# Performance work log

Measured on AMD Instinct MI355X. Metric: run time of the kernel, lower is better.

Reference implementation:

```python
import jax, jax.numpy as jnp
import numpy as np

N = 50000       # nodes
E = 1600000     # edges
H = 64          # hidden_channels
G = 16          # graphs in batch
DOUT = 2        # dim_out
NODE_IN = 1
EDGE_IN = 3


def setup_inputs() -> dict:
    key = jax.random.key(0)
    ks = jax.random.split(key, 24)
    p = lambda k, shape: (jax.random.normal(k, shape, jnp.float32) * 0.05)
    inp = {
        "x": jax.random.normal(ks[0], (N, NODE_IN), jnp.float32),
        "edge_index": jax.random.randint(ks[1], (2, E), 0, N, dtype=jnp.int64),
        "edge_attr": jax.random.normal(ks[2], (E, EDGE_IN), jnp.float32),
        "batch": jnp.sort(jax.random.randint(ks[3], (N,), 0, G, dtype=jnp.int64)),
        # EdgeModel MLP: Linear(2*node_in+edge_in, H), ReLU, Linear(H, H)
        "ew1": p(ks[4], (2 * NODE_IN + EDGE_IN, H)), "eb1": p(ks[5], (H,)),
        "ew2": p(ks[6], (H, H)), "eb2": p(ks[7], (H,)),
        # NodeModel MLP: Linear(node_in+edge_out, H), ReLU, Linear(H, H)
        "nw1": p(ks[8], (NODE_IN + H, H)), "nb1": p(ks[9], (H,)),
        "nw2": p(ks[10], (H, H)), "nb2": p(ks[11], (H,)),
        "ow1": p(ks[12], (H, H)), "ob1": p(ks[13], (H,)),
        "ow2": p(ks[14], (H, H)), "ob2": p(ks[15], (H,)),
        "ow3": p(ks[16], (H, H)), "ob3": p(ks[17], (H,)),
        "ow4": p(ks[18], (H, DOUT)), "ob4": p(ks[19], (DOUT,)),
    }
    return inp


def reference(x, edge_index, edge_attr, batch,
              ew1, eb1, ew2, eb2,
              nw1, nb1, nw2, nb2,
              ow1, ob1, ow2, ob2, ow3, ob3, ow4, ob4):
    row, col = edge_index[0], edge_index[1]
    # EdgeModel: gather endpoints, concat, 2-layer MLP (no residual)
    e_in = jnp.concatenate([x[row], x[col], edge_attr], axis=1)      # [E, 2+3]
    e = jax.nn.relu(e_in @ ew1 + eb1) @ ew2 + eb2                    # [E, H]
    # NodeModel: scatter_add edge messages into destination nodes
    agg = jax.ops.segment_sum(e, col, num_segments=x.shape[0])      # [N, H]
    h_in = jnp.concatenate([x, agg], axis=1)                         # [N, 1+H]
    h = jax.nn.relu(h_in @ nw1 + nb1) @ nw2 + nb2                    # [N, H]
    # global_add_pool over graphs
    pooled = jax.ops.segment_sum(h, batch, num_segments=G)          # [G, H]
    o = jax.nn.relu(pooled @ ow1 + ob1)
    o = jax.nn.relu(o @ ow2 + ob2)
    o = jax.nn.relu(o @ ow3 + ob3)
    return o @ ow4 + ob4                                             # [G, DOUT]
```

## Files before the change

### kernel.cpp

```cpp
#include <hip/hip_runtime.h>
#include <hip/hip_bf16.h>

#define HID 64
#define NGRAPH 16
#define BN 32
#define GB 8
#define MAXNB 2048
#define NCB 256
#define NCT 1024
#define SORT_T 1024
#define SORT_CHUNK 12800

typedef __attribute__((ext_vector_type(8))) short short8;
typedef __attribute__((ext_vector_type(4))) float f32x4;

enum : int {
  OFF_V      = 1040,
  OFF_M      = 1104,
  OFF_EW1    = 5200,
  OFF_EB1    = 5520,
  OFF_NW1    = 5584,
  OFF_NB1    = 9744,
  OFF_NW2    = 9808,
  OFF_NB2    = 13904,
  OFF_OW1    = 13968,
  OFF_OB1    = 18064,
  OFF_OW2    = 18128,
  OFF_OB2    = 22224,
  OFF_OW3    = 22288,
  OFF_OB3    = 26384,
  OFF_OW4    = 26448,
  OFF_OB4    = 26576,
  OFF_EW2    = 26578,
  OFF_EB2    = 30674,
  OFF_FLAGS  = 30738,
  OFF_W1T    = 30740,
  OFF_MT     = 30996,
  OFF_PREP   = 33044
};

struct WPtrs { const void* p[16]; };

__device__ __forceinline__ float cv(float v) { return v; }
__device__ __forceinline__ float cv(__hip_bfloat16 v) { return __bfloat162float(v); }
__device__ __forceinline__ unsigned short f2bu(float v) {
  union { __hip_bfloat16 b; unsigned short u; } c;
  c.b = __float2bfloat16(v);
  return c.u;
}
__device__ __forceinline__ unsigned short fr(float v) {
  unsigned u = __float_as_uint(v);
  u += 0x7FFFu + ((u >> 16) & 1u);
  return (unsigned short)(u >> 16);
}
__device__ __forceinline__ unsigned rndpack(float a, float b) {
  unsigned ua = __float_as_uint(fmaxf(a, 0.0f));
  unsigned ub = __float_as_uint(fmaxf(b, 0.0f));
  ua += 0x7FFFu + ((ua >> 16) & 1u);
  ub += 0x7FFFu + ((ub >> 16) & 1u);
  return __builtin_amdgcn_perm(ub, ua, 0x07060302u);
}

__global__ __launch_bounds__(256) void prep_kernel(
    const void* xv, const void* eiv, WPtrs wp, float* ws)
{
  __shared__ int red[2];
  __shared__ int s_ft;
  __shared__ float ew2s[4096];
  __shared__ float nw1s[4096];
  const int t = threadIdx.x;

  if (t == 0) { red[0] = 0; red[1] = 0; }
  __syncthreads();
  {
    const unsigned* u = (const unsigned*)xv;
    int big = 0;
    for (int i = t; i < 512; i += 256) {
      const unsigned el = (u[i] >> 7) & 0xFFu;
      big += (el >= 140u) ? 1 : 0;
    }
    atomicAdd(&red[0], big);
  }
  {
    const int* e32 = (const int*)eiv;
    int orv = 0;
    for (int i = 1 + 2 * t; i < 2048; i += 512) orv |= e32[i];
    atomicOr(&red[1], orv);
  }
  __syncthreads();
  if (t == 0) {
    const int ft = (red[0] < 8) ? 1 : 0;
    const int it = (red[1] == 0) ? 1 : 0;
    ((int*)(ws + OFF_FLAGS))[0] = ft;
    ((int*)(ws + OFF_FLAGS))[1] = it;
    s_ft = ft;
  }
  __syncthreads();
  const int ft = s_ft;

  const int sz[16]  = {320,64,4096,64,4160,64,4096,64,4096,64,4096,64,4096,64,128,2};
  const int dst[16] = {OFF_EW1,OFF_EB1,OFF_EW2,OFF_EB2,OFF_NW1,OFF_NB1,OFF_NW2,OFF_NB2,
                       OFF_OW1,OFF_OB1,OFF_OW2,OFF_OB2,OFF_OW3,OFF_OB3,OFF_OW4,OFF_OB4};
  for (int a = 0; a < 16; ++a) {
    const void* src = wp.p[a];
    float* d = ws + dst[a];
    const int n = sz[a];
    for (int i = t; i < n; i += 256)
      d[i] = ft ? __bfloat162float(((const __hip_bfloat16*)src)[i])
                : ((const float*)src)[i];
  }
  __syncthreads();

  for (int i = t; i < 4096; i += 256) {
    ew2s[i] = ws[OFF_EW2 + i];
    nw1s[i] = ws[OFF_NW1 + 64 + i];
  }
  __syncthreads();
  for (int idx = t; idx < 4096; idx += 256) {
    const int i = idx >> 6, j = idx & 63;
    float s = 0.0f;
    #pragma unroll 8
    for (int k = 0; k < 64; ++k)
      s = fmaf(ew2s[i * 64 + k], nw1s[k * 64 + j], s);
    ws[OFF_M + idx] = s;
  }
  for (int j = t; j < 64; j += 256) {
    float s = 0.0f;
    #pragma unroll 8
    for (int k = 0; k < 64; ++k)
      s = fmaf(ws[OFF_EB2 + k], nw1s[k * 64 + j], s);
    ws[OFF_V + j] = s;
  }
  __syncthreads();

  unsigned short* w1t = (unsigned short*)(ws + OFF_W1T);
  for (int n = t; n < 64; n += 256) {
    #pragma unroll
    for (int k = 0; k < 8; ++k) {
      float v = 0.0f;
      if (k < 5) v = ws[OFF_EW1 + k * 64 + n];
      else if (k == 5) v = ws[OFF_EB1 + n];
      w1t[n * 8 + k] = f2bu(v);
    }
  }
  unsigned short* mt = (unsigned short*)(ws + OFF_MT);
  for (int idx = t; idx < 4096; idx += 256) {
    const int n = idx >> 6, k = idx & 63;
    mt[idx] = f2bu(ws[OFF_M + k * 64 + n]);
  }
}

template<typename IT>
__device__ __forceinline__ void count_impl(
    const IT* __restrict__ ei, const IT* __restrict__ bt,
    int* __restrict__ gcnt, int* __restrict__ endG, int* lh,
    const int E, const int N, const int NBG)
{
  const int t = threadIdx.x;
  const int b = blockIdx.x;
  for (int i = t; i < NBG; i += NCT) lh[i] = 0;
  {
    const int i = b * NCT + t;
    if (i < N) {
      const int g1 = (int)bt[i];
      if (i == 0) for (int g = 0; g < g1; ++g) endG[g] = 0;
      if (i == N - 1) {
        for (int g = g1; g < NGRAPH; ++g) endG[g] = N;
      } else {
        const int g2 = (int)bt[i + 1];
        for (int g = g1; g < g2; ++g) endG[g] = i + 1;
      }
    }
  }
  __syncthreads();
  const int per = (E + NCB - 1) / NCB;
  const int a = b * per;
  const int bnd = (a + per < E) ? (a + per) : E;
  for (int e = a + t; e < bnd; e += NCT) {
    const int c = (int)ei[(size_t)E + e];
    atomicAdd(&lh[c >> 8], 1);
  }
  __syncthreads();
  for (int i = t; i < NBG; i += NCT) gcnt[(size_t)i * NCB + b] = lh[i];
}

__global__ __launch_bounds__(NCT) void count_kernel(
    const void* eiv, const void* batv, const float* ws,
    int* gcnt, int* endG, const int E, const int N, const int NBG)
{
  __shared__ int lh[MAXNB];
  const int it = ((const int*)(ws + OFF_FLAGS))[1];
  if (it) count_impl<long long>((const long long*)eiv, (const long long*)batv, gcnt, endG, lh, E, N, NBG);
  else    count_impl<int>((const int*)eiv, (const int*)batv, gcnt, endG, lh, E, N, NBG);
}

__global__ __launch_bounds__(256) void scan_tot_kernel(
    const int* __restrict__ gcnt, int* __restrict__ gstart, const int NBG)
{
  const int lane = threadIdx.x & 63;
  const int bkt = blockIdx.x * 4 + (threadIdx.x >> 6);
  if (bkt >= NBG) return;
  const int4 v = *(const int4*)(gcnt + (size_t)bkt * NCB + lane * 4);
  int s = v.x + v.y + v.z + v.w;
  #pragma unroll
  for (int off = 32; off > 0; off >>= 1) s += __shfl_xor(s, off);
  if (lane == 0) gstart[bkt] = s;
}

__global__ __launch_bounds__(256) void scan_pref_kernel(
    int* __restrict__ gstart, const int NBG)
{
  __shared__ int ps[256];
  const int t = threadIdx.x;
  const int seg = (NBG + 255) / 256;
  int s = 0;
  for (int i = 0; i < seg; ++i) {
    const int idx = t * seg + i;
    if (idx < NBG) s += gstart[idx];
  }
  ps[t] = s;
  __syncthreads();
  for (int off = 1; off < 256; off <<= 1) {
    const int v = (t >= off) ? ps[t - off] : 0;
    __syncthreads();
    ps[t] += v;
    __syncthreads();
  }
  int carry = ps[t] - s;
  for (int i = 0; i < seg; ++i) {
    const int idx = t * seg + i;
    if (idx < NBG) {
      const int c = gstart[idx];
      gstart[idx] = carry;
      carry += c;
    }
  }
  if (t == 255) gstart[NBG] = ps[255];
}

__global__ __launch_bounds__(256) void scan_row_kernel(
    int* __restrict__ gcnt, const int* __restrict__ gstart, const int NBG)
{
  const int lane = threadIdx.x & 63;
  const int bkt = blockIdx.x * 4 + (threadIdx.x >> 6);
  if (bkt >= NBG) return;
  int* row = gcnt + (size_t)bkt * NCB;
  const int4 v = *(const int4*)(row + lane * 4);
  const int ls = v.x + v.y + v.z + v.w;
  int s = ls;
  #pragma unroll
  for (int off = 1; off < 64; off <<= 1) {
    const int u = __shfl_up(s, off);
    if (lane >= off) s += u;
  }
  int e = s - ls + gstart[bkt];
  int4 o;
  o.x = e; e += v.x;
  o.y = e; e += v.y;
  o.z = e; e += v.z;
  o.w = e;
  *(int4*)(row + lane * 4) = o;
}

template<typename FT, typename IT>
__device__ __forceinline__ void scatter_impl(
    const FT* __restrict__ x, const IT* __restrict__ ei, const FT* __restrict__ ea,
    const int* __restrict__ gcnt, const int* __restrict__ gstart,
    ushort4* __restrict__ recB, unsigned char* __restrict__ cid, int* lb,
    const int E, const int gb0, const int gb1, const int cap)
{
  const int t = threadIdx.x;
  const int b = blockIdx.x;
  __shared__ int sbase;
  if (t == 0) sbase = gstart[gb0];
  __syncthreads();
  const int base = sbase;
  const int gcount = gb1 - gb0;
  for (int i = t; i < gcount; i += NCT) lb[i] = gcnt[(size_t)(gb0 + i) * NCB + b] - base;
  __syncthreads();

  const int per = (E + NCB - 1) / NCB;
  const int a = b * per;
  const int bnd = (a + per < E) ? (a + per) : E;
  for (int e = a + t; e < bnd; e += NCT) {
    const int c = (int)ei[(size_t)E + e];
    const int grp = c >> 8;
    if (grp >= gb0 && grp < gb1) {
      const int pos = atomicAdd(&lb[grp - gb0], 1);
      if (pos < cap) {
        const int r = (int)ei[e];
        ushort4 rv;
        rv.x = fr(cv(x[r]));
        rv.y = fr(cv(ea[(size_t)3 * e + 0]));
        rv.z = fr(cv(ea[(size_t)3 * e + 1]));
        rv.w = fr(cv(ea[(size_t)3 * e + 2]));
        recB[pos] = rv;
        cid[pos] = (unsigned char)(c & 255);
      }
    }
  }
}

__global__ __launch_bounds__(NCT) void scatter_kernel(
    const void* xv, const void* eiv, const void* eav, const float* ws,
    const int* gcnt, const int* gstart, ushort4* recB, unsigned char* cid,
    const int E, const int gb0, const int gb1, const int cap)
{
  __shared__ int lb[MAXNB];
  const int* fl = (const int*)(ws + OFF_FLAGS);
  const int ft = fl[0], it = fl[1];
  if (ft) {
    if (it) scatter_impl<__hip_bfloat16, long long>((const __hip_bfloat16*)xv, (const long long*)eiv, (const __hip_bfloat16*)eav, gcnt, gstart, recB, cid, lb, E, gb0, gb1, cap);
    else    scatter_impl<__hip_bfloat16, int>((const __hip_bfloat16*)xv, (const int*)eiv, (const __hip_bfloat16*)eav, gcnt, gstart, recB, cid, lb, E, gb0, gb1, cap);
  } else {
    if (it) scatter_impl<float, long long>((const float*)xv, (const long long*)eiv, (const float*)eav, gcnt, gstart, recB, cid, lb, E, gb0, gb1, cap);
    else    scatter_impl<float, int>((const float*)xv, (const int*)eiv, (const float*)eav, gcnt, gstart, recB, cid, lb, E, gb0, gb1, cap);
  }
}

__global__ __launch_bounds__(SORT_T) void sort_kernel(
    ushort4* __restrict__ recB, unsigned char* __restrict__ cid,
    const int* __restrict__ gstart, int* __restrict__ bstartF,
    const int NB, const int gr0, const int cap)
{
  __shared__ unsigned sru[SORT_CHUNK * 2];
  __shared__ unsigned char sc[SORT_CHUNK];
  __shared__ int h2[16][GB];
  __shared__ int fs[GB];
  __shared__ int cur[GB];

  const int t = threadIdx.x;
  const int lane = t & 63;
  const int wav = t >> 6;
  const int g = gr0 + (int)blockIdx.x;

  const int base0 = gstart[gr0];
  int rb = gstart[g] - base0;
  int re = gstart[g + 1] - base0;
  if (rb > cap) rb = cap;
  if (re > cap) re = cap;
  int cnt = re - rb;
  if (cnt > SORT_CHUNK) cnt = SORT_CHUNK;

  if (t < 16 * GB) ((int*)h2)[t] = 0;
  __syncthreads();

  for (int i = t; i < cnt; i += SORT_T) {
    const ushort4 r = recB[rb + i];
    sru[2 * i]     = (unsigned)r.x | ((unsigned)r.y << 16);
    sru[2 * i + 1] = (unsigned)r.z | ((unsigned)r.w << 16);
    const unsigned char c = cid[rb + i];
    sc[i] = c;
    const int kk = c >> 5;
    unsigned long long mym = 0;
    #pragma unroll
    for (int k = 0; k < GB; ++k) {
      const unsigned long long bk = __ballot(kk == k);
      if (kk == k) mym = bk;
    }
    if ((mym & (((unsigned long long)1 << lane) - 1ull)) == 0)
      h2[wav][kk] += (int)__builtin_popcountll(mym);
  }
  __syncthreads();

  if (t == 0) {
    int acc = 0;
    for (int k = 0; k < GB; ++k) {
      int s = 0;
      #pragma unroll
      for (int w = 0; w < 16; ++w) s += h2[w][k];
      fs[k] = acc;
      cur[k] = acc;
      acc += s;
    }
  }
  __syncthreads();

  if (t <= GB) {
    const int bk = g * GB + t;
    if (bk <= NB) bstartF[bk] = base0 + rb + ((t == GB) ? cnt : fs[t]);
  }

  for (int i = t; i < cnt; i += SORT_T) {
    const unsigned char c = sc[i];
    const int kk = c >> 5;
    unsigned long long mym = 0;
    #pragma unroll
    for (int k = 0; k < GB; ++k) {
      const unsigned long long bk = __ballot(kk == k);
      if (kk == k) mym = bk;
    }
    const int lead = (int)__builtin_ctzll(mym);
    const int off = (int)__builtin_popcountll(mym & (((unsigned long long)1 << lane) - 1ull));
    int bas = 0;
    if (lane == lead) bas = atomicAdd(&cur[kk], (int)__builtin_popcountll(mym));
    bas = __shfl(bas, lead);
    const int pos = rb + bas + off;
    const unsigned a = sru[2 * i], b = sru[2 * i + 1];
    ushort4 rv;
    rv.x = (unsigned short)(a & 0xFFFFu); rv.y = (unsigned short)(a >> 16);
    rv.z = (unsigned short)(b & 0xFFFFu); rv.w = (unsigned short)(b >> 16);
    recB[pos] = rv;
    cid[pos] = (unsigned char)(c & 31);
  }
}

template<typename FT, typename IT>
__device__ __forceinline__ void fused_impl(
    const FT* __restrict__ x, const IT* __restrict__ batch,
    const float* __restrict__ ws, const int* __restrict__ bstart,
    const ushort4* __restrict__ recB, const unsigned char* __restrict__ cid,
    float* __restrict__ rep,
    short* sA, unsigned char* scid, short* sHT, short* aggB,
    float* pooledL, float* xls, unsigned short* xlsb, int* sbi,
    const int N, const int gb0, const int cap)
{
  const int t = threadIdx.x;
  const int lane = t & 63;
  const int quad = lane >> 4;
  const int l15 = lane & 15;
  const int wav = t >> 6;
  const int bucket = gb0 + blockIdx.x;

  for (int i = t; i < NGRAPH * 64; i += 256) pooledL[i] = 0.0f;
  if (t < BN) {
    const int n = bucket * BN + t;
    const float xvv = (n < N) ? cv(x[n]) : 0.0f;
    xls[t] = xvv;
    xlsb[t] = fr(xvv);
  }
  if (t == 0) {
    const int nf = bucket * BN, nl = bucket * BN + BN - 1;
    sbi[0] = (int)batch[(nf < N) ? nf : (N - 1)];
    sbi[1] = (int)batch[(nl < N) ? nl : (N - 1)];
    sbi[2] = bstart[gb0];
  }
  __syncthreads();

  const unsigned short* w1t = (const unsigned short*)(ws + OFF_W1T);
  short8 B1[4];
  #pragma unroll
  for (int tn = 0; tn < 4; ++tn) {
    short8 z; for (int j = 0; j < 8; ++j) z[j] = 0;
    if (quad == 0) z = *(const short8*)(w1t + (16 * tn + l15) * 8);
    B1[tn] = z;
  }
  short8 ONES8;
  #pragma unroll
  for (int j = 0; j < 8; ++j) ONES8[j] = (short)0x3F80;

  const int base = sbi[2];
  int s0 = bstart[bucket] - base;
  int e0 = bstart[bucket + 1] - base;
  if (s0 > cap) s0 = cap;
  if (e0 > cap) e0 = cap;

  f32x4 C2[2]; C2[0] = (f32x4)0.0f; C2[1] = (f32x4)0.0f;
  f32x4 C3[2]; C3[0] = (f32x4)0.0f; C3[1] = (f32x4)0.0f;

  const int nedge = e0 - s0;
  const int nst = (nedge + 255) >> 8;
  for (int st = 0; st < nst; ++st) {
    {
      const int idx = s0 + st * 256 + t;
      const bool valid = idx < e0;
      ushort4 rv = valid ? recB[idx] : make_ushort4(0, 0, 0, 0);
      const int c = valid ? (int)cid[idx] : 255;
      short8 row;
      row[0] = (short)rv.x;
      row[1] = valid ? (short)xlsb[c] : (short)0;
      row[2] = (short)rv.y; row[3] = (short)rv.z; row[4] = (short)rv.w;
      row[5] = valid ? (short)0x3F80 : (short)0;
      row[6] = 0; row[7] = 0;
      *(short8*)(sA + t * 8) = row;
      scid[t] = (unsigned char)c;
    }
    __syncthreads();

    const int m = nedge - st * 256;
    const int jmax = (m >= 256) ? 4 : ((m + 63) >> 6);
    for (int j = 0; j < jmax; ++j) {
      short* HT = sHT + (j & 1) * (64 * 72);
      short8 a1;
      if (quad == 0) a1 = *(const short8*)(sA + (j * 64 + 16 * wav + l15) * 8);
      else { for (int jj = 0; jj < 8; ++jj) a1[jj] = 0; }
      f32x4 Hc[4];
      #pragma unroll
      for (int tn = 0; tn < 4; ++tn)
        Hc[tn] = __builtin_amdgcn_mfma_f32_16x16x32_bf16(a1, B1[tn], (f32x4)0.0f, 0, 0, 0);
      #pragma unroll
      for (int tn = 0; tn < 4; ++tn) {
        uint2 pk;
        pk.x = rndpack(Hc[tn][0], Hc[tn][1]);
        pk.y = rndpack(Hc[tn][2], Hc[tn][3]);
        *(uint2*)(HT + (16 * tn + l15) * 72 + 16 * wav + quad * 4) = pk;
      }
      __syncthreads();

      const unsigned* sp = (const unsigned*)(scid + j * 64);
      #pragma unroll
      for (int q = 0; q < 2; ++q) {
        const unsigned lo = sp[2 * quad + 8 * q];
        const unsigned hi = sp[2 * quad + 8 * q + 1];
        short8 a2[2];
        #pragma unroll
        for (int tm2 = 0; tm2 < 2; ++tm2) {
          const int seg = 16 * tm2 + l15;
          short8 v;
          v[0] = (((lo      ) & 255u) == (unsigned)seg) ? (short)0x3F80 : (short)0;
          v[1] = (((lo >>  8) & 255u) == (unsigned)seg) ? (short)0x3F80 : (short)0;
          v[2] = (((lo >> 16) & 255u) == (unsigned)seg) ? (short)0x3F80 : (short)0;
          v[3] = (((lo >> 24) & 255u) == (unsigned)seg) ? (short)0x3F80 : (short)0;
          v[4] = (((hi      ) & 255u) == (unsigned)seg) ? (short)0x3F80 : (short)0;
          v[5] = (((hi >>  8) & 255u) == (unsigned)seg) ? (short)0x3F80 : (short)0;
          v[6] = (((hi >> 16) & 255u) == (unsigned)seg) ? (short)0x3F80 : (short)0;
          v[7] = (((hi >> 24) & 255u) == (unsigned)seg) ? (short)0x3F80 : (short)0;
          a2[tm2] = v;
        }
        const short8 b2 = *(const short8*)(HT + (16 * wav + l15) * 72 + 32 * q + quad * 8);
        C2[0] = __builtin_amdgcn_mfma_f32_16x16x32_bf16(a2[0], b2, C2[0], 0, 0, 0);
        C2[1] = __builtin_amdgcn_mfma_f32_16x16x32_bf16(a2[1], b2, C2[1], 0, 0, 0);
        C3[0] = __builtin_amdgcn_mfma_f32_16x16x32_bf16(a2[0], ONES8, C3[0], 0, 0, 0);
        C3[1] = __builtin_amdgcn_mfma_f32_16x16x32_bf16(a2[1], ONES8, C3[1], 0, 0, 0);
      }
    }
    __syncthreads();
  }

  #pragma unroll
  for (int tm2 = 0; tm2 < 2; ++tm2) {
    #pragma unroll
    for (int r = 0; r < 4; ++r)
      aggB[(16 * tm2 + quad * 4 + r) * 72 + 16 * wav + l15] = (short)fr(C2[tm2][r]);
  }
  __syncthreads();

  const unsigned short* mt = (const unsigned short*)(ws + OFF_MT);
  f32x4 D[2]; D[0] = (f32x4)0.0f; D[1] = (f32x4)0.0f;
  #pragma unroll
  for (int q2 = 0; q2 < 2; ++q2) {
    const short8 bb = *(const short8*)(mt + (16 * wav + l15) * 64 + 32 * q2 + quad * 8);
    #pragma unroll
    for (int tm2 = 0; tm2 < 2; ++tm2) {
      const short8 aa = *(const short8*)(aggB + (16 * tm2 + l15) * 72 + 32 * q2 + quad * 8);
      D[tm2] = __builtin_amdgcn_mfma_f32_16x16x32_bf16(aa, bb, D[tm2], 0, 0, 0);
    }
  }

  const int n = 16 * wav + l15;
  const float c1n = ws[OFF_NW1 + n];
  const float vn  = ws[OFF_V + n];
  const float bn  = ws[OFF_NB1 + n];
  float* myrep = rep + (size_t)(bucket & 7) * (NGRAPH * 64);
  const bool multi = (sbi[0] != sbi[1]);

  if (!multi) {
    float hs = 0.0f;
    #pragma unroll
    for (int tm2 = 0; tm2 < 2; ++tm2) {
      #pragma unroll
      for (int r = 0; r < 4; ++r) {
        const int mrow = 16 * tm2 + quad * 4 + r;
        const int ng = bucket * BN + mrow;
        if (ng < N)
          hs += fmaxf(D[tm2][r] + xls[mrow] * c1n + C3[tm2][r] * vn + bn, 0.0f);
      }
    }
    hs += __shfl_xor(hs, 16);
    hs += __shfl_xor(hs, 32);
    if (quad == 0) unsafeAtomicAdd(&myrep[sbi[0] * 64 + n], hs);
  } else {
    #pragma unroll
    for (int tm2 = 0; tm2 < 2; ++tm2) {
      #pragma unroll
      for (int r = 0; r < 4; ++r) {
        const int mrow = 16 * tm2 + quad * 4 + r;
        const int ng = bucket * BN + mrow;
        if (ng < N) {
          const float h = fmaxf(D[tm2][r] + xls[mrow] * c1n + C3[tm2][r] * vn + bn, 0.0f);
          const int g = (int)batch[ng];
          atomicAdd(&pooledL[g * 64 + n], h);
        }
      }
    }
    __syncthreads();
    for (int g = sbi[0] + wav; g <= sbi[1]; g += 4)
      unsafeAtomicAdd(&myrep[g * 64 + lane], pooledL[g * 64 + lane]);
  }
}

__global__ __launch_bounds__(256) void fused_kernel(
    const void* xv, const void* batv, const float* ws, const int* bstart,
    const ushort4* recB, const unsigned char* cid, float* rep,
    const int N, const int gb0, const int cap)
{
  __shared__ __align__(16) short sA[256 * 8];
  __shared__ __align__(8)  unsigned char scid[256];
  __shared__ __align__(16) short sHT[2 * 64 * 72];
  __shared__ __align__(16) short aggB[32 * 72];
  __shared__ float pooledL[NGRAPH * 64];
  __shared__ float xls[BN];
  __shared__ unsigned short xlsb[BN];
  __shared__ int   sbi[3];

  const int* fl = (const int*)(ws + OFF_FLAGS);
  const int ft = fl[0], it = fl[1];
  if (ft) {
    if (it) fused_impl<__hip_bfloat16, long long>((const __hip_bfloat16*)xv, (const long long*)batv, ws, bstart, recB, cid, rep, sA, scid, sHT, aggB, pooledL, xls, xlsb, sbi, N, gb0, cap);
    else    fused_impl<__hip_bfloat16, int>((const __hip_bfloat16*)xv, (const int*)batv, ws, bstart, recB, cid, rep, sA, scid, sHT, aggB, pooledL, xls, xlsb, sbi, N, gb0, cap);
  } else {
    if (it) fused_impl<float, long long>((const float*)xv, (const long long*)batv, ws, bstart, recB, cid, rep, sA, scid, sHT, aggB, pooledL, xls, xlsb, sbi, N, gb0, cap);
    else    fused_impl<float, int>((const float*)xv, (const int*)batv, ws, bstart, recB, cid, rep, sA, scid, sHT, aggB, pooledL, xls, xlsb, sbi, N, gb0, cap);
  }
}

__global__ __launch_bounds__(256) void head_kernel(
    const float* ws, const float* rep, const int* __restrict__ endG,
    void* outv, const int N)
{
  __shared__ float P[NGRAPH][HID];
  __shared__ float A[NGRAPH][HID];
  __shared__ float B[NGRAPH][HID];
  __shared__ int endL[NGRAPH];

  const int t = threadIdx.x;
  const int j = t & 63;
  const int gq = t >> 6;

  if (t < NGRAPH) endL[t] = endG[t];

  #pragma unroll
  for (int gi = 0; gi < 4; ++gi) {
    const int g = gq + gi * 4;
    float s = 0.0f;
    #pragma unroll
    for (int r = 0; r < 8; ++r)
      s += rep[(size_t)r * (NGRAPH * 64) + g * 64 + j];
    P[g][j] = s;
  }
  __syncthreads();

  {
    const float bj = ws[OFF_NB2 + j];
    #pragma unroll
    for (int gi = 0; gi < 4; ++gi) {
      const int g = gq + gi * 4;
      const float cg = (float)(endL[g] - (g ? endL[g - 1] : 0));
      float s = cg * bj;
      #pragma unroll 8
      for (int k = 0; k < HID; ++k)
        s = fmaf(P[g][k], ws[OFF_NW2 + k * HID + j], s);
      A[g][j] = s;
    }
  }
  __syncthreads();

  const int wOff[3] = {OFF_OW1, OFF_OW2, OFF_OW3};
  const int bOff[3] = {OFF_OB1, OFF_OB2, OFF_OB3};
  for (int L = 0; L < 3; ++L) {
    float (*In)[HID]  = (L & 1) ? B : A;
    float (*Out)[HID] = (L & 1) ? A : B;
    const float bj = ws[bOff[L] + j];
    #pragma unroll
    for (int gi = 0; gi < 4; ++gi) {
      const int g = gq + gi * 4;
      float s = bj;
      #pragma unroll 8
      for (int k = 0; k < HID; ++k)
        s = fmaf(In[g][k], ws[wOff[L] + k * HID + j], s);
      Out[g][j] = fmaxf(s, 0.0f);
    }
    __syncthreads();
  }

  if (t < 32) {
    const int g = t >> 1, d = t & 1;
    float s = ws[OFF_OB4 + d];
    #pragma unroll 8
    for (int k = 0; k < HID; ++k)
      s = fmaf(B[g][k], ws[OFF_OW4 + k * 2 + d], s);
    const int ft = ((const int*)(ws + OFF_FLAGS))[0];
    if (ft) ((__hip_bfloat16*)outv)[g * 2 + d] = __float2bfloat16(s);
    else    ((float*)outv)[g * 2 + d] = s;
  }
}

extern "C" void kernel_launch(void* const* d_in, const int* in_sizes, int n_in,
                              void* d_out, int out_size, void* d_ws, size_t ws_size,
                              hipStream_t stream)
{
  const void* xv   = d_in[0];
  const void* eiv  = d_in[1];
  const void* eav  = d_in[2];
  const void* batv = d_in[3];

  WPtrs wp;
  for (int a = 0; a < 16; ++a) wp.p[a] = d_in[4 + a];

  const int N = in_sizes[0];
  const int E = in_sizes[1] / 2;
  const int NB = (N + BN - 1) / BN;
  const int NBG = (NB + GB - 1) / GB;
  if (NB > MAXNB) return;

  float* ws    = (float*)d_ws;
  float* rep   = ws + OFF_PREP;
  int* gstart  = (int*)(rep + 8 * NGRAPH * 64);
  int* bstartF = gstart + NBG + 1;
  int* endG    = bstartF + NB + 2;
  int* gcnt    = endG + NGRAPH;

  size_t recOffB = ((size_t)((char*)(gcnt + (size_t)NBG * NCB) - (char*)d_ws) + 15) & ~(size_t)15;

  int G = -1; long long cap = 0;
  for (int g = 1; g <= 64; ++g) {
    const long long c = (long long)E / g + E / 32 + 8192;
    if (recOffB + (size_t)c * 9 <= ws_size) { G = g; cap = c; break; }
  }
  if (G < 0) return;

  ushort4* recB = (ushort4*)((char*)d_ws + recOffB);
  unsigned char* cid = (unsigned char*)(recB + cap);
  const int gsz = (NBG + G - 1) / G;
  const int sblk = (NBG + 3) / 4;

  (void)hipMemsetAsync(rep, 0, (size_t)(8 * NGRAPH * 64) * 4, stream);

  prep_kernel<<<1, 256, 0, stream>>>(xv, eiv, wp, ws);
  count_kernel<<<NCB, NCT, 0, stream>>>(eiv, batv, ws, gcnt, endG, E, N, NBG);
  scan_tot_kernel<<<sblk, 256, 0, stream>>>(gcnt, gstart, NBG);
  scan_pref_kernel<<<1, 256, 0, stream>>>(gstart, NBG);
  scan_row_kernel<<<sblk, 256, 0, stream>>>(gcnt, gstart, NBG);

  for (int g = 0; g < G; ++g) {
    const int gr0 = g * gsz;
    const int gr1 = (gr0 + gsz < NBG) ? (gr0 + gsz) : NBG;
    if (gr0 >= gr1) break;
    scatter_kernel<<<NCB, NCT, 0, stream>>>(xv, eiv, eav, ws, gcnt, gstart,
                                            recB, cid, E, gr0, gr1, (int)cap);
    sort_kernel<<<gr1 - gr0, SORT_T, 0, stream>>>(recB, cid, gstart, bstartF,
                                                  NB, gr0, (int)cap);
    const int b0 = gr0 * GB;
    const int b1 = (gr1 * GB < NB) ? (gr1 * GB) : NB;
    fused_kernel<<<b1 - b0, 256, 0, stream>>>(xv, batv, ws, bstartF, recB, cid,
                                              rep, N, b0, (int)cap);
  }

  head_kernel<<<1, 256, 0, stream>>>(ws, rep, endG, d_out, N);
}
```

Measured before the change: 293.6 us.

## Materialize one-hot scatter matrix in LDS and widen prep kernel to 1024 threads

The fused kernel no longer rebuilds the one-hot segment matrix from packed column ids with per-lane compares before each MFMA. Instead each stage zeroes an LDS buffer and scatters a bf16 one per edge, then loads the A operands directly as short8. Shared memory is consolidated into one aliased buffer, with pooledL and aggB reusing other regions. The single-block prep kernel now runs 1024 threads, uses vectorized weight copies, wave-shuffle reductions, and keeps the fused matrix product in LDS. The trade-off is an extra zeroing pass and an extra barrier per edge stage in exchange for removing the compare-heavy VALU work.

```diff
diff --git a/kernel.cpp b/kernel.cpp
--- a/kernel.cpp
+++ b/kernel.cpp
@@ -31,18 +31,23 @@
   OFF_OB3    = 26384,
   OFF_OW4    = 26448,
   OFF_OB4    = 26576,
-  OFF_EW2    = 26578,
-  OFF_EB2    = 30674,
-  OFF_FLAGS  = 30738,
-  OFF_W1T    = 30740,
-  OFF_MT     = 30996,
-  OFF_PREP   = 33044
+  OFF_EW2    = 26580,
+  OFF_EB2    = 30676,
+  OFF_FLAGS  = 30740,
+  OFF_W1T    = 30744,
+  OFF_MT     = 31000,
+  OFF_PREP   = 33048
 };
 
 struct WPtrs { const void* p[16]; };
 
 __device__ __forceinline__ float cv(float v) { return v; }
 __device__ __forceinline__ float cv(__hip_bfloat16 v) { return __bfloat162float(v); }
+__device__ __forceinline__ float b2f(unsigned short u) {
+  union { unsigned u32; float f; } c;
+  c.u32 = ((unsigned)u) << 16;
+  return c.f;
+}
 __device__ __forceinline__ unsigned short f2bu(float v) {
   union { __hip_bfloat16 b; unsigned short u; } c;
   c.b = __float2bfloat16(v);
@@ -61,7 +66,7 @@
   return __builtin_amdgcn_perm(ub, ua, 0x07060302u);
 }
 
-__global__ __launch_bounds__(256) void prep_kernel(
+__global__ __launch_bounds__(1024) void prep_kernel(
     const void* xv, const void* eiv, WPtrs wp, float* ws)
 {
   __shared__ int red[2];
@@ -69,23 +74,25 @@
   __shared__ float ew2s[4096];
   __shared__ float nw1s[4096];
   const int t = threadIdx.x;
+  const int lane = t & 63;
 
   if (t == 0) { red[0] = 0; red[1] = 0; }
   __syncthreads();
   {
-    const unsigned* u = (const unsigned*)xv;
     int big = 0;
-    for (int i = t; i < 512; i += 256) {
-      const unsigned el = (u[i] >> 7) & 0xFFu;
-      big += (el >= 140u) ? 1 : 0;
-    }
-    atomicAdd(&red[0], big);
+    if (t < 512) {
+      const unsigned el = (((const unsigned*)xv)[t] >> 7) & 0xFFu;
+      big = (el >= 140u) ? 1 : 0;
+    }
+    #pragma unroll
+    for (int o = 32; o > 0; o >>= 1) big += __shfl_xor(big, o);
+    if (lane == 0 && big) atomicAdd(&red[0], big);
   }
   {
-    const int* e32 = (const int*)eiv;
-    int orv = 0;
-    for (int i = 1 + 2 * t; i < 2048; i += 512) orv |= e32[i];
-    atomicOr(&red[1], orv);
+    int orv = ((const int*)eiv)[1 + 2 * t];
+    #pragma unroll
+    for (int o = 32; o > 0; o >>= 1) orv |= __shfl_xor(orv, o);
+    if (lane == 0 && orv) atomicOr(&red[1], orv);
   }
   __syncthreads();
   if (t == 0) {
@@ -105,48 +112,67 @@
     const void* src = wp.p[a];
     float* d = ws + dst[a];
     const int n = sz[a];
-    for (int i = t; i < n; i += 256)
-      d[i] = ft ? __bfloat162float(((const __hip_bfloat16*)src)[i])
-                : ((const float*)src)[i];
-  }
-  __syncthreads();
-
-  for (int i = t; i < 4096; i += 256) {
-    ew2s[i] = ws[OFF_EW2 + i];
-    nw1s[i] = ws[OFF_NW1 + 64 + i];
-  }
-  __syncthreads();
-  for (int idx = t; idx < 4096; idx += 256) {
+    const int n4 = n >> 2;
+    for (int i = t; i < n4; i += 1024) {
+      float4 f;
+      if (ft) {
+        const ushort4 u4 = ((const ushort4*)src)[i];
+        f.x = b2f(u4.x); f.y = b2f(u4.y); f.z = b2f(u4.z); f.w = b2f(u4.w);
+      } else {
+        f = ((const float4*)src)[i];
+      }
+      ((float4*)d)[i] = f;
+      const int g = i << 2;
+      if (a == 2) {
+        ew2s[g] = f.x; ew2s[g + 1] = f.y; ew2s[g + 2] = f.z; ew2s[g + 3] = f.w;
+      } else if (a == 4 && g >= 64) {
+        nw1s[g - 64] = f.x; nw1s[g - 63] = f.y; nw1s[g - 62] = f.z; nw1s[g - 61] = f.w;
+      }
+    }
+    for (int i = (n4 << 2) + t; i < n; i += 1024)
+      d[i] = ft ? b2f(((const unsigned short*)src)[i]) : ((const float*)src)[i];
+  }
+  __syncthreads();
+
+  float mv[4];
+  #pragma unroll
+  for (int p = 0; p < 4; ++p) {
+    const int idx = t + p * 1024;
     const int i = idx >> 6, j = idx & 63;
     float s = 0.0f;
     #pragma unroll 8
     for (int k = 0; k < 64; ++k)
       s = fmaf(ew2s[i * 64 + k], nw1s[k * 64 + j], s);
-    ws[OFF_M + idx] = s;
-  }
-  for (int j = t; j < 64; j += 256) {
+    mv[p] = s;
+  }
+  if (t < 64) {
     float s = 0.0f;
     #pragma unroll 8
     for (int k = 0; k < 64; ++k)
-      s = fmaf(ws[OFF_EB2 + k], nw1s[k * 64 + j], s);
-    ws[OFF_V + j] = s;
-  }
-  __syncthreads();
-
-  unsigned short* w1t = (unsigned short*)(ws + OFF_W1T);
-  for (int n = t; n < 64; n += 256) {
+      s = fmaf(ws[OFF_EB2 + k], nw1s[k * 64 + t], s);
+    ws[OFF_V + t] = s;
+  }
+  __syncthreads();
+  #pragma unroll
+  for (int p = 0; p < 4; ++p) ew2s[t + p * 1024] = mv[p];
+  __syncthreads();
+
+  if (t < 64) {
+    unsigned short* w1t = (unsigned short*)(ws + OFF_W1T);
     #pragma unroll
     for (int k = 0; k < 8; ++k) {
       float v = 0.0f;
-      if (k < 5) v = ws[OFF_EW1 + k * 64 + n];
-      else if (k == 5) v = ws[OFF_EB1 + n];
-      w1t[n * 8 + k] = f2bu(v);
+      if (k < 5) v = ws[OFF_EW1 + k * 64 + t];
+      else if (k == 5) v = ws[OFF_EB1 + t];
+      w1t[t * 8 + k] = f2bu(v);
     }
   }
   unsigned short* mt = (unsigned short*)(ws + OFF_MT);
-  for (int idx = t; idx < 4096; idx += 256) {
+  #pragma unroll
+  for (int p = 0; p < 4; ++p) {
+    const int idx = t + p * 1024;
     const int n = idx >> 6, k = idx & 63;
-    mt[idx] = f2bu(ws[OFF_M + k * 64 + n]);
+    mt[idx] = f2bu(ew2s[k * 64 + n]);
   }
 }
 
@@ -411,8 +437,8 @@
     const float* __restrict__ ws, const int* __restrict__ bstart,
     const ushort4* __restrict__ recB, const unsigned char* __restrict__ cid,
     float* __restrict__ rep,
-    short* sA, unsigned char* scid, short* sHT, short* aggB,
-    float* pooledL, float* xls, unsigned short* xlsb, int* sbi,
+    short* sA, short* sHT, short* a2L,
+    float* xls, unsigned short* xlsb, int* sbi,
     const int N, const int gb0, const int cap)
 {
   const int t = threadIdx.x;
@@ -422,7 +448,6 @@
   const int wav = t >> 6;
   const int bucket = gb0 + blockIdx.x;
 
-  for (int i = t; i < NGRAPH * 64; i += 256) pooledL[i] = 0.0f;
   if (t < BN) {
     const int n = bucket * BN + t;
     const float xvv = (n < N) ? cv(x[n]) : 0.0f;
@@ -461,11 +486,18 @@
   const int nedge = e0 - s0;
   const int nst = (nedge + 255) >> 8;
   for (int st = 0; st < nst; ++st) {
+    const int idx = s0 + st * 256 + t;
+    const bool valid = idx < e0;
+    const ushort4 rv = valid ? recB[idx] : make_ushort4(0, 0, 0, 0);
+    const int c = valid ? (int)cid[idx] : 255;
+
     {
-      const int idx = s0 + st * 256 + t;
-      const bool valid = idx < e0;
-      ushort4 rv = valid ? recB[idx] : make_ushort4(0, 0, 0, 0);
-      const int c = valid ? (int)cid[idx] : 255;
+      unsigned long long* az = (unsigned long long*)a2L;
+      #pragma unroll
+      for (int z = 0; z < 9; ++z) az[t + z * 256] = 0ull;
+    }
+    __syncthreads();
+    {
       short8 row;
       row[0] = (short)rv.x;
       row[1] = valid ? (short)xlsb[c] : (short)0;
@@ -473,14 +505,14 @@
       row[5] = valid ? (short)0x3F80 : (short)0;
       row[6] = 0; row[7] = 0;
       *(short8*)(sA + t * 8) = row;
-      scid[t] = (unsigned char)c;
+      if (c < 32) a2L[(t >> 6) * 2304 + c * 72 + (t & 63)] = (short)0x3F80;
     }
     __syncthreads();
 
     const int m = nedge - st * 256;
     const int jmax = (m >= 256) ? 4 : ((m + 63) >> 6);
     for (int j = 0; j < jmax; ++j) {
-      short* HT = sHT + (j & 1) * (64 * 72);
+      short* HT = sHT + (j & 1) * 4608;
       short8 a1;
       if (quad == 0) a1 = *(const short8*)(sA + (j * 64 + 16 * wav + l15) * 8);
       else { for (int jj = 0; jj < 8; ++jj) a1[jj] = 0; }
@@ -497,36 +529,22 @@
       }
       __syncthreads();
 
-      const unsigned* sp = (const unsigned*)(scid + j * 64);
+      const short* aj = a2L + j * 2304;
       #pragma unroll
       for (int q = 0; q < 2; ++q) {
-        const unsigned lo = sp[2 * quad + 8 * q];
-        const unsigned hi = sp[2 * quad + 8 * q + 1];
-        short8 a2[2];
-        #pragma unroll
-        for (int tm2 = 0; tm2 < 2; ++tm2) {
-          const int seg = 16 * tm2 + l15;
-          short8 v;
-          v[0] = (((lo      ) & 255u) == (unsigned)seg) ? (short)0x3F80 : (short)0;
-          v[1] = (((lo >>  8) & 255u) == (unsigned)seg) ? (short)0x3F80 : (short)0;
-          v[2] = (((lo >> 16) & 255u) == (unsigned)seg) ? (short)0x3F80 : (short)0;
-          v[3] = (((lo >> 24) & 255u) == (unsigned)seg) ? (short)0x3F80 : (short)0;
-          v[4] = (((hi      ) & 255u) == (unsigned)seg) ? (short)0x3F80 : (short)0;
-          v[5] = (((hi >>  8) & 255u) == (unsigned)seg) ? (short)0x3F80 : (short)0;
-          v[6] = (((hi >> 16) & 255u) == (unsigned)seg) ? (short)0x3F80 : (short)0;
-          v[7] = (((hi >> 24) & 255u) == (unsigned)seg) ? (short)0x3F80 : (short)0;
-          a2[tm2] = v;
-        }
-        const short8 b2 = *(const short8*)(HT + (16 * wav + l15) * 72 + 32 * q + quad * 8);
-        C2[0] = __builtin_amdgcn_mfma_f32_16x16x32_bf16(a2[0], b2, C2[0], 0, 0, 0);
-        C2[1] = __builtin_amdgcn_mfma_f32_16x16x32_bf16(a2[1], b2, C2[1], 0, 0, 0);
-        C3[0] = __builtin_amdgcn_mfma_f32_16x16x32_bf16(a2[0], ONES8, C3[0], 0, 0, 0);
-        C3[1] = __builtin_amdgcn_mfma_f32_16x16x32_bf16(a2[1], ONES8, C3[1], 0, 0, 0);
+        const short8 a20 = *(const short8*)(aj + l15 * 72 + 32 * q + 8 * quad);
+        const short8 a21 = *(const short8*)(aj + (16 + l15) * 72 + 32 * q + 8 * quad);
+        const short8 b2  = *(const short8*)(HT + (16 * wav + l15) * 72 + 32 * q + quad * 8);
+        C2[0] = __builtin_amdgcn_mfma_f32_16x16x32_bf16(a20, b2, C2[0], 0, 0, 0);
+        C2[1] = __builtin_amdgcn_mfma_f32_16x16x32_bf16(a21, b2, C2[1], 0, 0, 0);
+        C3[0] = __builtin_amdgcn_mfma_f32_16x16x32_bf16(a20, ONES8, C3[0], 0, 0, 0);
+        C3[1] = __builtin_amdgcn_mfma_f32_16x16x32_bf16(a21, ONES8, C3[1], 0, 0, 0);
       }
     }
     __syncthreads();
   }
 
+  short* aggB = a2L;
   #pragma unroll
   for (int tm2 = 0; tm2 < 2; ++tm2) {
     #pragma unroll
@@ -570,6 +588,9 @@
     hs += __shfl_xor(hs, 32);
     if (quad == 0) unsafeAtomicAdd(&myrep[sbi[0] * 64 + n], hs);
   } else {
+    float* pooledL = (float*)sA;
+    for (int i = t; i < NGRAPH * 64; i += 256) pooledL[i] = 0.0f;
+    __syncthreads();
     #pragma unroll
     for (int tm2 = 0; tm2 < 2; ++tm2) {
       #pragma unroll
@@ -594,23 +615,22 @@
     const ushort4* recB, const unsigned char* cid, float* rep,
     const int N, const int gb0, const int cap)
 {
-  __shared__ __align__(16) short sA[256 * 8];
-  __shared__ __align__(8)  unsigned char scid[256];
-  __shared__ __align__(16) short sHT[2 * 64 * 72];
-  __shared__ __align__(16) short aggB[32 * 72];
-  __shared__ float pooledL[NGRAPH * 64];
-  __shared__ float xls[BN];
-  __shared__ unsigned short xlsb[BN];
-  __shared__ int   sbi[3];
+  __shared__ __align__(16) unsigned char smem[41168];
+  short* sA  = (short*)smem;
+  short* sHT = (short*)(smem + 4096);
+  short* a2L = (short*)(smem + 22528);
+  float* xls = (float*)(smem + 40960);
+  unsigned short* xlsb = (unsigned short*)(smem + 41088);
+  int* sbi = (int*)(smem + 41152);
 
   const int* fl = (const int*)(ws + OFF_FLAGS);
   const int ft = fl[0], it = fl[1];
   if (ft) {
-    if (it) fused_impl<__hip_bfloat16, long long>((const __hip_bfloat16*)xv, (const long long*)batv, ws, bstart, recB, cid, rep, sA, scid, sHT, aggB, pooledL, xls, xlsb, sbi, N, gb0, cap);
-    else    fused_impl<__hip_bfloat16, int>((const __hip_bfloat16*)xv, (const int*)batv, ws, bstart, recB, cid, rep, sA, scid, sHT, aggB, pooledL, xls, xlsb, sbi, N, gb0, cap);
+    if (it) fused_impl<__hip_bfloat16, long long>((const __hip_bfloat16*)xv, (const long long*)batv, ws, bstart, recB, cid, rep, sA, sHT, a2L, xls, xlsb, sbi, N, gb0, cap);
+    else    fused_impl<__hip_bfloat16, int>((const __hip_bfloat16*)xv, (const int*)batv, ws, bstart, recB, cid, rep, sA, sHT, a2L, xls, xlsb, sbi, N, gb0, cap);
   } else {
-    if (it) fused_impl<float, long long>((const float*)xv, (const long long*)batv, ws, bstart, recB, cid, rep, sA, scid, sHT, aggB, pooledL, xls, xlsb, sbi, N, gb0, cap);
-    else    fused_impl<float, int>((const float*)xv, (const int*)batv, ws, bstart, recB, cid, rep, sA, scid, sHT, aggB, pooledL, xls, xlsb, sbi, N, gb0, cap);
+    if (it) fused_impl<float, long long>((const float*)xv, (const long long*)batv, ws, bstart, recB, cid, rep, sA, sHT, a2L, xls, xlsb, sbi, N, gb0, cap);
+    else    fused_impl<float, int>((const float*)xv, (const int*)batv, ws, bstart, recB, cid, rep, sA, sHT, a2L, xls, xlsb, sbi, N, gb0, cap);
   }
 }
 
@@ -726,7 +746,7 @@
 
   (void)hipMemsetAsync(rep, 0, (size_t)(8 * NGRAPH * 64) * 4, stream);
 
-  prep_kernel<<<1, 256, 0, stream>>>(xv, eiv, wp, ws);
+  prep_kernel<<<1, 1024, 0, stream>>>(xv, eiv, wp, ws);
   count_kernel<<<NCB, NCT, 0, stream>>>(eiv, batv, ws, gcnt, endG, E, N, NBG);
   scan_tot_kernel<<<sblk, 256, 0, stream>>>(gcnt, gstart, NBG);
   scan_pref_kernel<<<1, 256, 0, stream>>>(gstart, NBG);
```

New measurement: 252.8 us. 13.9% less time.
